# Performance work log

Hardware: AMD Instinct MI355X
Metric: run time of the kernel (lower is better)

Reference implementation:

```python
import jax, jax.numpy as jnp
import numpy as np

D_MODEL = 2048
N_HEADS = 16
D_HEAD = D_MODEL // N_HEADS
D_FF = 8192
EPS = 1e-6
ROPE_BASE = 10000.0


def rmsnorm(x, g):
    return x * jax.lax.rsqrt(jnp.mean(x * x, axis=-1, keepdims=True) + EPS) * g


def rotate_half(x):
    x1, x2 = jnp.split(x, 2, axis=-1)
    return jnp.concatenate((-x2, x1), axis=-1)


def rope_tables(T):
    inv_freq = 1.0 / (ROPE_BASE ** (jnp.arange(0, D_HEAD, 2, dtype=jnp.float32) / D_HEAD))
    freqs = jnp.arange(T, dtype=jnp.float32)[:, None] * inv_freq[None, :]  # [T, D_HEAD//2]
    emb = jnp.concatenate((freqs, freqs), axis=-1)  # [T, D_HEAD]
    return jnp.cos(emb), jnp.sin(emb)


def setup_inputs() -> dict:
    key = jax.random.key(0)
    ks = jax.random.split(key, 6)
    std = 0.02
    x = jax.random.normal(ks[0], (2, 2048, D_MODEL), dtype=jnp.float32)
    # weights stored (in, out) so forward is x @ W
    w_qkv = jax.random.normal(ks[1], (D_MODEL, 3 * D_MODEL), dtype=jnp.float32) * std
    w_out = jax.random.normal(ks[2], (D_MODEL, D_MODEL), dtype=jnp.float32) * std
    w_g = jax.random.normal(ks[3], (D_MODEL, D_FF), dtype=jnp.float32) * std
    w_u = jax.random.normal(ks[4], (D_MODEL, D_FF), dtype=jnp.float32) * std
    w_o = jax.random.normal(ks[5], (D_FF, D_MODEL), dtype=jnp.float32) * std
    g1 = jnp.ones((D_MODEL,), dtype=jnp.float32)
    g2 = jnp.ones((D_MODEL,), dtype=jnp.float32)
    return {"x": x, "w_qkv": w_qkv, "w_out": w_out, "g1": g1, "g2": g2,
            "w_g": w_g, "w_u": w_u, "w_o": w_o}


def reference(x, w_qkv, w_out, g1, g2, w_g, w_u, w_o):
    B, T, D = x.shape
    H, dh = N_HEADS, D_HEAD
    scale = dh ** -0.5

    h = rmsnorm(x, g1)
    qkv = h @ w_qkv  # [B, T, 3D]
    q, k, v = jnp.split(qkv, 3, axis=-1)
    # [B, H, T, dh]
    q = q.reshape(B, T, H, dh).transpose(0, 2, 1, 3)
    k = k.reshape(B, T, H, dh).transpose(0, 2, 1, 3)
    v = v.reshape(B, T, H, dh).transpose(0, 2, 1, 3)

    cos, sin = rope_tables(T)  # [T, dh] each
    cos = cos[None, None]
    sin = sin[None, None]
    q = q * cos + rotate_half(q) * sin
    k = k * cos + rotate_half(k) * sin

    scores = jnp.einsum('bhqd,bhkd->bhqk', q, k) * scale
    causal = jnp.arange(T)[None, :] <= jnp.arange(T)[:, None]  # [T, T]
    scores = jnp.where(causal[None, None], scores, -jnp.inf)
    attn = jax.nn.softmax(scores, axis=-1)
    ctx = jnp.einsum('bhqk,bhkd->bhqd', attn, v)  # [B, H, T, dh]
    ctx = ctx.transpose(0, 2, 1, 3).reshape(B, T, D)
    x = x + ctx @ w_out

    h = rmsnorm(x, g2)
    x = x + (jax.nn.silu(h @ w_g) * (h @ w_u)) @ w_o
    return x
```

## Files before the change

### kernel.cpp

```cpp
#include <hip/hip_runtime.h>

typedef __bf16 bf16x8 __attribute__((ext_vector_type(8)));
typedef float f32x4 __attribute__((ext_vector_type(4)));
typedef unsigned short u16x8 __attribute__((ext_vector_type(8)));

#define B_SZ 2
#define T_SEQ 2048
#define D_MODEL 2048
#define N_HEADS 16
#define D_HEAD 128
#define D_FF 8192
#define BT (B_SZ * T_SEQ)
#define NT (T_SEQ / 64)

__device__ __forceinline__ unsigned short f2bf(float f) {
  unsigned int u = __builtin_bit_cast(unsigned int, f);
  u += 0x7FFFu + ((u >> 16) & 1u);
  return (unsigned short)(u >> 16);
}
__device__ __forceinline__ float bf2f(unsigned short h) {
  unsigned int u = ((unsigned int)h) << 16;
  return __builtin_bit_cast(float, u);
}

__device__ __forceinline__ void load_lds16(const void* g, void* l) {
  __builtin_amdgcn_global_load_lds(
      (const __attribute__((address_space(1))) unsigned int*)g,
      (__attribute__((address_space(3))) unsigned int*)l, 16, 0, 0);
}

__global__ __launch_bounds__(256) void transpose_cast_kernel(
    const float* __restrict__ in, unsigned short* __restrict__ out, int R, int C) {
  __shared__ float tile[32][33];
  const int tx = threadIdx.x, ty = threadIdx.y;
  const int c0 = blockIdx.x * 32, r0 = blockIdx.y * 32;
#pragma unroll
  for (int i = 0; i < 4; ++i)
    tile[ty + 8 * i][tx] = in[(long)(r0 + ty + 8 * i) * C + c0 + tx];
  __syncthreads();
#pragma unroll
  for (int i = 0; i < 4; ++i)
    out[(long)(c0 + ty + 8 * i) * R + r0 + tx] = f2bf(tile[tx][ty + 8 * i]);
}

__global__ __launch_bounds__(256) void rmsnorm_cast_kernel(
    const float* __restrict__ x, const float* __restrict__ gw,
    unsigned short* __restrict__ out) {
  const int row = blockIdx.x;
  const int tid = threadIdx.x;
  const float* xr = x + (long)row * D_MODEL;
  float4 a = *(const float4*)(xr + tid * 8);
  float4 b = *(const float4*)(xr + tid * 8 + 4);
  float ss = a.x * a.x + a.y * a.y + a.z * a.z + a.w * a.w +
             b.x * b.x + b.y * b.y + b.z * b.z + b.w * b.w;
#pragma unroll
  for (int d = 1; d < 64; d <<= 1) ss += __shfl_xor(ss, d);
  __shared__ float part[4];
  if ((tid & 63) == 0) part[tid >> 6] = ss;
  __syncthreads();
  ss = part[0] + part[1] + part[2] + part[3];
  const float rs = rsqrtf(ss * (1.0f / D_MODEL) + 1e-6f);
  float4 g0 = *(const float4*)(gw + tid * 8);
  float4 g1 = *(const float4*)(gw + tid * 8 + 4);
  ushort4 o0, o1;
  o0.x = f2bf(a.x * rs * g0.x); o0.y = f2bf(a.y * rs * g0.y);
  o0.z = f2bf(a.z * rs * g0.z); o0.w = f2bf(a.w * rs * g0.w);
  o1.x = f2bf(b.x * rs * g1.x); o1.y = f2bf(b.y * rs * g1.y);
  o1.z = f2bf(b.z * rs * g1.z); o1.w = f2bf(b.w * rs * g1.w);
  unsigned short* op = out + (long)row * D_MODEL + tid * 8;
  *(ushort4*)op = o0;
  *(ushort4*)(op + 4) = o1;
}

template <int EPI>
__global__ __launch_bounds__(256) void gemm_bt_kernel(
    const unsigned short* __restrict__ A, const unsigned short* __restrict__ Bt,
    void* __restrict__ Cout, const void* __restrict__ aux,
    int M, int N, int K, int lda, int ldb, int ldc) {
  __shared__ unsigned short As[128 * 32];
  __shared__ unsigned short Bs[128 * 32];
  const int tid = threadIdx.x;
  const int w = tid >> 6, lane = tid & 63, g = lane >> 4, c = lane & 15;
  const int m0 = blockIdx.y * 128, n0 = blockIdx.x * 128;
  const int wm = (w >> 1) * 64, wn = (w & 1) * 64;
  const int srow = lane >> 2;
  const int scol = (lane & 3) * 8;
  const int ch0 = w * 2;
  f32x4 acc[4][4] = {};
  const int nkt = K >> 5;
  const unsigned short* Abase = A + (long)m0 * lda + scol;
  const unsigned short* Bbase = Bt + (long)n0 * ldb + scol;
  for (int kt = 0; kt < nkt; ++kt) {
    __syncthreads();
#pragma unroll
    for (int i = 0; i < 2; ++i) {
      const int ch = ch0 + i;
      load_lds16(Abase + (long)(ch * 16 + srow) * lda + kt * 32, &As[ch * 512]);
      load_lds16(Bbase + (long)(ch * 16 + srow) * ldb + kt * 32, &Bs[ch * 512]);
    }
    __syncthreads();
    bf16x8 fa[4], fb[4];
#pragma unroll
    for (int m = 0; m < 4; ++m)
      fa[m] = *(const bf16x8*)(As + (wm + m * 16 + c) * 32 + g * 8);
#pragma unroll
    for (int n = 0; n < 4; ++n)
      fb[n] = *(const bf16x8*)(Bs + (wn + n * 16 + c) * 32 + g * 8);
#pragma unroll
    for (int m = 0; m < 4; ++m)
#pragma unroll
      for (int n = 0; n < 4; ++n)
        acc[m][n] = __builtin_amdgcn_mfma_f32_16x16x32_bf16(fa[m], fb[n], acc[m][n], 0, 0, 0);
  }
#pragma unroll
  for (int m = 0; m < 4; ++m) {
#pragma unroll
    for (int r = 0; r < 4; ++r) {
      const int row = m0 + wm + m * 16 + 4 * g + r;
#pragma unroll
      for (int n = 0; n < 4; ++n) {
        const int col = n0 + wn + n * 16 + c;
        const long idx = (long)row * ldc + col;
        float v = acc[m][n][r];
        if constexpr (EPI == 0) {
          ((unsigned short*)Cout)[idx] = f2bf(v);
        } else if constexpr (EPI == 1) {
          ((float*)Cout)[idx] = v + ((const float*)aux)[idx];
        } else {
          const float u = bf2f(((const unsigned short*)aux)[idx]);
          const float s = v / (1.0f + __expf(-v));
          ((unsigned short*)Cout)[idx] = f2bf(s * u);
        }
      }
    }
  }
}

template <int EPI, int WM, int WN, int FM, int FN>
__global__ __launch_bounds__(WM * WN * 64, 2) void gemm_ks_kernel(
    const unsigned short* __restrict__ A, const unsigned short* __restrict__ Bt,
    void* __restrict__ Cout, const void* __restrict__ aux,
    int M, int N, int K, int lda, int ldb, int ldc, int cm, int cn) {
  constexpr int THREADS = WM * WN * 64;
  constexpr int BM = WM * FM * 16;
  constexpr int BN = WN * FN * 16;
  constexpr int ASLOT = BM * 32;
  constexpr int BSLOT = BN * 32;
  constexpr int RPR = THREADS / 4;
  __shared__ unsigned short As[4 * ASLOT];
  __shared__ unsigned short Bs[4 * BSLOT];

  const int tid = threadIdx.x;
  const int lane = tid & 63, g = lane >> 4, c = lane & 15;
  const int w = tid >> 6, wr = w / WN, wc = w % WN;

  const int nbn = N / BN;
  const int bid = (int)blockIdx.x;
  const int xcd = bid & 7, idx = bid >> 3;
  const int chn = nbn / cn;
  const int crow = xcd / chn, ccol = xcd % chn;
  const int mr = idx / cn, nc2 = idx % cn;
  const int m0 = (crow * cm + mr) * BM;
  const int n0 = (ccol * cn + nc2) * BN;

  const int nks = K >> 5;
  const int srow = tid >> 2;
  const int kq8 = (tid & 3) * 8;
  const unsigned short* A_ = A + (long)m0 * lda;
  const unsigned short* B_ = Bt + (long)n0 * ldb;

  auto stage = [&](int s) {
    const int slot = s & 3;
    const long kofs = (long)s * 32 + kq8;
#pragma unroll
    for (int j = 0; j < BM / RPR; ++j)
      load_lds16(A_ + (long)(j * RPR + srow) * lda + kofs,
                 &As[slot * ASLOT + (j * THREADS + tid) * 8]);
#pragma unroll
    for (int j = 0; j < BN / RPR; ++j)
      load_lds16(B_ + (long)(j * RPR + srow) * ldb + kofs,
                 &Bs[slot * BSLOT + (j * THREADS + tid) * 8]);
  };

  f32x4 acc[FM][FN] = {};

  stage(0);
  if (nks > 1) stage(1);
  if (nks > 2) stage(2);
  asm volatile("s_waitcnt vmcnt(8)" ::: "memory");
  __builtin_amdgcn_sched_barrier(0);
  __builtin_amdgcn_s_barrier();

  for (int s = 0; s < nks; ++s) {
    const int slot = s & 3;
    const unsigned short* Ap = &As[slot * ASLOT] + (wr * FM * 16 + c) * 32 + g * 8;
    const unsigned short* Bp = &Bs[slot * BSLOT] + (wc * FN * 16 + c) * 32 + g * 8;
    bf16x8 fa[FM], fb[FN];
#pragma unroll
    for (int fm = 0; fm < FM; ++fm) fa[fm] = *(const bf16x8*)(Ap + fm * 512);
#pragma unroll
    for (int fn = 0; fn < FN; ++fn) fb[fn] = *(const bf16x8*)(Bp + fn * 512);
    if (s + 3 < nks) stage(s + 3);
    __builtin_amdgcn_s_setprio(1);
#pragma unroll
    for (int fm = 0; fm < FM; ++fm)
#pragma unroll
      for (int fn = 0; fn < FN; ++fn)
        acc[fm][fn] = __builtin_amdgcn_mfma_f32_16x16x32_bf16(fa[fm], fb[fn], acc[fm][fn], 0, 0, 0);
    __builtin_amdgcn_s_setprio(0);
    if (s + 1 == nks) break;
    if (s <= nks - 4)
      asm volatile("s_waitcnt vmcnt(8)" ::: "memory");
    else if (s == nks - 3)
      asm volatile("s_waitcnt vmcnt(4)" ::: "memory");
    else
      asm volatile("s_waitcnt vmcnt(0)" ::: "memory");
    __builtin_amdgcn_sched_barrier(0);
    __builtin_amdgcn_s_barrier();
  }

#pragma unroll
  for (int fm = 0; fm < FM; ++fm) {
#pragma unroll
    for (int r = 0; r < 4; ++r) {
      const int row = m0 + wr * FM * 16 + fm * 16 + 4 * g + r;
#pragma unroll
      for (int fn = 0; fn < FN; ++fn) {
        const int col = n0 + wc * FN * 16 + fn * 16 + c;
        const long idx2 = (long)row * ldc + col;
        float v = acc[fm][fn][r];
        if constexpr (EPI == 0) {
          ((unsigned short*)Cout)[idx2] = f2bf(v);
        } else if constexpr (EPI == 1) {
          ((float*)Cout)[idx2] = v + ((const float*)aux)[idx2];
        } else {
          const float u = bf2f(((const unsigned short*)aux)[idx2]);
          const float sg = v / (1.0f + __expf(-v));
          ((unsigned short*)Cout)[idx2] = f2bf(sg * u);
        }
      }
    }
  }
}

__global__ void rope_tables_kernel(float* __restrict__ cost, float* __restrict__ sint) {
  const int idx = blockIdx.x * 256 + threadIdx.x;
  const int t = idx >> 6, i = idx & 63;
  const float invf = powf(10000.0f, -(float)i * (1.0f / 64.0f));
  const float ang = (float)t * invf;
  cost[idx] = cosf(ang);
  sint[idx] = sinf(ang);
}

__global__ __launch_bounds__(256) void rope_apply_kernel(
    unsigned short* __restrict__ qkv, const float* __restrict__ cost,
    const float* __restrict__ sint) {
  const long idx = (long)blockIdx.x * 256 + threadIdx.x;
  const int i = idx & 63;
  const int h = (idx >> 6) & 15;
  const int qk = (idx >> 10) & 1;
  const int row = idx >> 11;
  const int t = row & (T_SEQ - 1);
  unsigned short* p = qkv + (long)row * (3 * D_MODEL) + qk * D_MODEL + h * D_HEAD + i;
  const float a = bf2f(p[0]);
  const float b = bf2f(p[64]);
  const float cv = cost[t * 64 + i];
  const float sv = sint[t * 64 + i];
  p[0] = f2bf(a * cv - b * sv);
  p[64] = f2bf(b * cv + a * sv);
}

__global__ __launch_bounds__(256) void vtrans_kernel(
    const unsigned short* __restrict__ qkv, unsigned short* __restrict__ vt) {
  __shared__ unsigned short tile[32][33];
  const int tx = threadIdx.x, ty = threadIdx.y;
  const int t0 = blockIdx.x * 32, d0 = blockIdx.y * 32;
  const int bh = blockIdx.z;
  const int b = bh >> 4, h = bh & 15;
#pragma unroll
  for (int i = 0; i < 4; ++i)
    tile[ty + 8 * i][tx] =
        qkv[(long)(b * T_SEQ + t0 + ty + 8 * i) * (3 * D_MODEL) + 2 * D_MODEL + h * D_HEAD + d0 + tx];
  __syncthreads();
#pragma unroll
  for (int i = 0; i < 4; ++i)
    vt[((long)bh * D_HEAD + d0 + ty + 8 * i) * T_SEQ + t0 + tx] = tile[tx][ty + 8 * i];
}

__global__ __launch_bounds__(256) void attn_kernel(
    const unsigned short* __restrict__ qkv, const unsigned short* __restrict__ vt,
    unsigned short* __restrict__ ctx) {
  __shared__ unsigned short Ks[2][64 * 128];
  __shared__ unsigned short Vs[2][128 * 64];
  const int h = blockIdx.y, b = blockIdx.z;
  const int tid = threadIdx.x;
  const int w = tid >> 6, lane = tid & 63, g = lane >> 4, c = lane & 15;
  const float scale = 0.08838834764831845f;
  const int srcA = (2 * (g & 1)) * 16 + c;
  const int srcB = srcA + 16;
  const bool hi = (g >> 1) != 0;
  const int bh = b * N_HEADS + h;

  const int ssk = (tid & 15) ^ ((tid >> 4) & 7);
  const int ssv = (tid & 7) ^ ((tid >> 3) & 7);
  const unsigned short* Kg = qkv + (long)b * T_SEQ * 3 * D_MODEL + D_MODEL + (long)h * D_HEAD;
  const unsigned short* Vg = vt + (long)bh * D_HEAD * T_SEQ;

  auto stage = [&](int kv0, int bufi) {
#pragma unroll
    for (int i = 0; i < 4; ++i) {
      const int rowk = i * 16 + (tid >> 4);
      load_lds16(Kg + (long)(kv0 + rowk) * (3 * D_MODEL) + ssk * 8,
                 &Ks[bufi][(i * 256 + tid) * 8]);
    }
#pragma unroll
    for (int i = 0; i < 4; ++i) {
      const int rowv = i * 32 + (tid >> 3);
      load_lds16(Vg + (long)rowv * T_SEQ + kv0 + ssv * 8,
                 &Vs[bufi][(i * 256 + tid) * 8]);
    }
  };

  const int cs7 = c & 7;

  for (int pass = 0; pass < 2; ++pass) {
    const int qt = pass ? (NT - 1 - blockIdx.x) : blockIdx.x;
    const int q = qt * 64 + w * 16 + c;

    bf16x8 fq[4];
    const long rowQ = (long)(b * T_SEQ + q) * (3 * D_MODEL) + h * D_HEAD;
#pragma unroll
    for (int ks = 0; ks < 4; ++ks)
      fq[ks] = *(const bf16x8*)(qkv + rowQ + ks * 32 + g * 8);

    f32x4 o[8] = {};
    float mrun = -INFINITY, ell = 0.0f;

    stage(0, 0);
    asm volatile("s_waitcnt vmcnt(0)" ::: "memory");
    __syncthreads();
    int buf = 0;

    for (int kt = 0; kt <= qt; ++kt) {
      const int kv0 = kt * 64;
      if (kt < qt) stage(kv0 + 64, buf ^ 1);

      f32x4 s[4] = {};
#pragma unroll
      for (int fm = 0; fm < 4; ++fm) {
        const unsigned short* kr = &Ks[buf][(fm * 16 + c) * 128];
#pragma unroll
        for (int ks = 0; ks < 4; ++ks) {
          bf16x8 ak = *(const bf16x8*)(kr + ((ks * 4 + g) ^ cs7) * 8);
          s[fm] = __builtin_amdgcn_mfma_f32_16x16x32_bf16(ak, fq[ks], s[fm], 0, 0, 0);
        }
      }
      float pmax = -INFINITY;
      const bool diag = (kt == qt);
#pragma unroll
      for (int fm = 0; fm < 4; ++fm)
#pragma unroll
        for (int r = 0; r < 4; ++r) {
          float sv = s[fm][r] * scale;
          if (diag) {
            const int kp = kv0 + fm * 16 + 4 * g + r;
            if (kp > q) sv = -INFINITY;
          }
          s[fm][r] = sv;
          pmax = fmaxf(pmax, sv);
        }
      pmax = fmaxf(pmax, __shfl_xor(pmax, 16));
      pmax = fmaxf(pmax, __shfl_xor(pmax, 32));
      const float mnew = fmaxf(mrun, pmax);
      const float resc = __expf(mrun - mnew);
      mrun = mnew;
      float rowsum = 0.0f;
#pragma unroll
      for (int fm = 0; fm < 4; ++fm)
#pragma unroll
        for (int r = 0; r < 4; ++r) {
          const float p = __expf(s[fm][r] - mnew);
          s[fm][r] = p;
          rowsum += p;
        }
      rowsum += __shfl_xor(rowsum, 16);
      rowsum += __shfl_xor(rowsum, 32);
      ell = ell * resc + rowsum;
#pragma unroll
      for (int fm = 0; fm < 8; ++fm) o[fm] *= resc;

      bf16x8 pb[2];
#pragma unroll
      for (int k2 = 0; k2 < 2; ++k2) {
        float va[4], vb[4];
#pragma unroll
        for (int r = 0; r < 4; ++r) {
          const float t0 = __shfl(s[k2 * 2][r], srcA);
          const float t1 = __shfl(s[k2 * 2 + 1][r], srcA);
          va[r] = hi ? t1 : t0;
          const float u0 = __shfl(s[k2 * 2][r], srcB);
          const float u1 = __shfl(s[k2 * 2 + 1][r], srcB);
          vb[r] = hi ? u1 : u0;
        }
        bf16x8 pv;
        pv[0] = (__bf16)va[0]; pv[1] = (__bf16)va[1];
        pv[2] = (__bf16)va[2]; pv[3] = (__bf16)va[3];
        pv[4] = (__bf16)vb[0]; pv[5] = (__bf16)vb[1];
        pv[6] = (__bf16)vb[2]; pv[7] = (__bf16)vb[3];
        pb[k2] = pv;
      }
#pragma unroll
      for (int fm = 0; fm < 8; ++fm) {
        const unsigned short* vr = &Vs[buf][(fm * 16 + c) * 64];
#pragma unroll
        for (int k2 = 0; k2 < 2; ++k2) {
          bf16x8 av = *(const bf16x8*)(vr + ((k2 * 4 + g) ^ cs7) * 8);
          o[fm] = __builtin_amdgcn_mfma_f32_16x16x32_bf16(av, pb[k2], o[fm], 0, 0, 0);
        }
      }
      asm volatile("s_waitcnt vmcnt(0)" ::: "memory");
      __syncthreads();
      buf ^= 1;
    }

    const float inv = 1.0f / ell;
    unsigned short* outp = ctx + (long)(b * T_SEQ + q) * D_MODEL + h * D_HEAD;
#pragma unroll
    for (int fm = 0; fm < 8; ++fm) {
      ushort4 pk;
      pk.x = f2bf(o[fm][0] * inv);
      pk.y = f2bf(o[fm][1] * inv);
      pk.z = f2bf(o[fm][2] * inv);
      pk.w = f2bf(o[fm][3] * inv);
      *(ushort4*)(outp + fm * 16 + 4 * g) = pk;
    }
  }
}

extern "C" void kernel_launch(void* const* d_in, const int* in_sizes, int n_in,
                              void* d_out, int out_size, void* d_ws, size_t ws_size,
                              hipStream_t stream) {
  const float* x = (const float*)d_in[0];
  const float* w_qkv = (const float*)d_in[1];
  const float* w_out = (const float*)d_in[2];
  const float* g1 = (const float*)d_in[3];
  const float* g2 = (const float*)d_in[4];
  const float* w_g = (const float*)d_in[5];
  const float* w_u = (const float*)d_in[6];
  const float* w_o = (const float*)d_in[7];
  float* out = (float*)d_out;

  char* ws = (char*)d_ws;
  size_t off = 0;
  auto take = [&](size_t bytes) {
    char* p = ws + off;
    off += (bytes + 255) & ~(size_t)255;
    return p;
  };

  char* Wreg = take((size_t)3 * D_FF * D_MODEL * 2);
  unsigned short* wTqkv = (unsigned short*)Wreg;
  unsigned short* wTout = (unsigned short*)(Wreg + (size_t)3 * D_MODEL * D_MODEL * 2);
  unsigned short* wTg = (unsigned short*)Wreg;
  unsigned short* wTu = (unsigned short*)(Wreg + (size_t)D_FF * D_MODEL * 2);
  unsigned short* wTo = (unsigned short*)(Wreg + (size_t)2 * D_FF * D_MODEL * 2);

  const size_t qkv_b = (size_t)BT * 3 * D_MODEL * 2;
  const size_t vt_b = (size_t)B_SZ * N_HEADS * D_HEAD * T_SEQ * 2;
  const size_t ctx_b = (size_t)BT * D_MODEL * 2;
  char* AR = take(qkv_b + vt_b + ctx_b);
  unsigned short* qkvb = (unsigned short*)AR;
  unsigned short* vtb = (unsigned short*)(AR + qkv_b);
  unsigned short* ctxb = (unsigned short*)(AR + qkv_b + vt_b);
  unsigned short* gbuf = (unsigned short*)AR;
  unsigned short* ubuf = (unsigned short*)(AR + (size_t)BT * (D_FF / 2) * 2);

  float* x1 = (float*)take((size_t)BT * D_MODEL * 4);
  unsigned short* hb = (unsigned short*)take((size_t)BT * D_MODEL * 2);
  float* cost = (float*)take((size_t)T_SEQ * 64 * 4);
  float* sint = (float*)take((size_t)T_SEQ * 64 * 4);

  const dim3 tb(32, 8);

  transpose_cast_kernel<<<dim3(3 * D_MODEL / 32, D_MODEL / 32), tb, 0, stream>>>(w_qkv, wTqkv, D_MODEL, 3 * D_MODEL);
  transpose_cast_kernel<<<dim3(D_MODEL / 32, D_MODEL / 32), tb, 0, stream>>>(w_out, wTout, D_MODEL, D_MODEL);
  rope_tables_kernel<<<T_SEQ * 64 / 256, 256, 0, stream>>>(cost, sint);

  rmsnorm_cast_kernel<<<BT, 256, 0, stream>>>(x, g1, hb);
  gemm_ks_kernel<0, 2, 4, 8, 4><<<384, 512, 0, stream>>>(
      hb, wTqkv, qkvb, nullptr, BT, 3 * D_MODEL, D_MODEL, D_MODEL, D_MODEL, 3 * D_MODEL, 8, 6);
  rope_apply_kernel<<<(BT * N_HEADS * 64 * 2) / 256, 256, 0, stream>>>(qkvb, cost, sint);
  vtrans_kernel<<<dim3(T_SEQ / 32, D_HEAD / 32, B_SZ * N_HEADS), tb, 0, stream>>>(qkvb, vtb);
  attn_kernel<<<dim3(NT / 2, N_HEADS, B_SZ), 256, 0, stream>>>(qkvb, vtb, ctxb);
  gemm_ks_kernel<1, 2, 2, 4, 4><<<512, 256, 0, stream>>>(
      ctxb, wTout, x1, x, BT, D_MODEL, D_MODEL, D_MODEL, D_MODEL, D_MODEL, 8, 8);

  transpose_cast_kernel<<<dim3(D_FF / 32, D_MODEL / 32), tb, 0, stream>>>(w_g, wTg, D_MODEL, D_FF);
  transpose_cast_kernel<<<dim3(D_FF / 32, D_MODEL / 32), tb, 0, stream>>>(w_u, wTu, D_MODEL, D_FF);
  transpose_cast_kernel<<<dim3(D_MODEL / 32, D_FF / 32), tb, 0, stream>>>(w_o, wTo, D_FF, D_MODEL);
  rmsnorm_cast_kernel<<<BT, 256, 0, stream>>>(x1, g2, hb);

  const int NH = D_FF / 2;
  for (int half = 0; half < 2; ++half) {
    const unsigned short* wTu_h = wTu + (size_t)half * NH * D_MODEL;
    const unsigned short* wTg_h = wTg + (size_t)half * NH * D_MODEL;
    const unsigned short* wTo_h = wTo + (size_t)half * NH;
    gemm_ks_kernel<0, 2, 4, 8, 4><<<256, 512, 0, stream>>>(
        hb, wTu_h, ubuf, nullptr, BT, NH, D_MODEL, D_MODEL, D_MODEL, NH, 4, 8);
    gemm_ks_kernel<2, 2, 4, 8, 4><<<256, 512, 0, stream>>>(
        hb, wTg_h, gbuf, ubuf, BT, NH, D_MODEL, D_MODEL, D_MODEL, NH, 4, 8);
    gemm_ks_kernel<1, 2, 2, 4, 4><<<512, 256, 0, stream>>>(
        gbuf, wTo_h, out, (half == 0) ? x1 : out, BT, D_MODEL, NH, NH, D_FF, D_MODEL, 8, 8);
  }
}
```

Baseline: 804.5 us.

## Add double-buffered 256x256 GEMM kernel with swizzled LDS for QKV and MLP

Replaces the unused gemm_bt kernel with a new 256x256-tile GEMM that uses 512 threads and a BK=64 double-buffered LDS pipeline. It prefetches two stages ahead with explicit vmcnt waits, XOR-swizzles LDS columns to avoid bank conflicts, and raises wave priority around the MFMA block. The QKV, up-projection and gate-projection GEMMs now call it with XCD-aware block mapping. The goal is to hide global load latency and reuse more data per tile, at the cost of 128 KB of LDS per block and heavy register pressure from 32 accumulators.

New measurement: 804.6 us. Within noise of the previous version (+0.0%).

```diff
diff --git a/kernel.cpp b/kernel.cpp
--- a/kernel.cpp
+++ b/kernel.cpp
@@ -73,55 +73,104 @@
 }
 
 template <int EPI>
-__global__ __launch_bounds__(256) void gemm_bt_kernel(
+__global__ __launch_bounds__(512, 2) void gemm256_kernel(
     const unsigned short* __restrict__ A, const unsigned short* __restrict__ Bt,
     void* __restrict__ Cout, const void* __restrict__ aux,
-    int M, int N, int K, int lda, int ldb, int ldc) {
-  __shared__ unsigned short As[128 * 32];
-  __shared__ unsigned short Bs[128 * 32];
+    int M, int N, int K, int lda, int ldb, int ldc, int cm, int cn) {
+  __shared__ unsigned short As[2][16384];
+  __shared__ unsigned short Bs[2][16384];
   const int tid = threadIdx.x;
-  const int w = tid >> 6, lane = tid & 63, g = lane >> 4, c = lane & 15;
-  const int m0 = blockIdx.y * 128, n0 = blockIdx.x * 128;
-  const int wm = (w >> 1) * 64, wn = (w & 1) * 64;
-  const int srow = lane >> 2;
-  const int scol = (lane & 3) * 8;
-  const int ch0 = w * 2;
-  f32x4 acc[4][4] = {};
-  const int nkt = K >> 5;
-  const unsigned short* Abase = A + (long)m0 * lda + scol;
-  const unsigned short* Bbase = Bt + (long)n0 * ldb + scol;
+  const int lane = tid & 63, g = lane >> 4, c = lane & 15;
+  const int w = tid >> 6, wr = w >> 2, wc = w & 3;
+
+  const int nbn = N >> 8;
+  const int bid = (int)blockIdx.x;
+  const int xcd = bid & 7, bidx = bid >> 3;
+  const int chn = nbn / cn;
+  const int crow = xcd / chn, ccol = xcd % chn;
+  const int m0 = (crow * cm + bidx / cn) << 8;
+  const int n0 = (ccol * cn + bidx % cn) << 8;
+
+  const int nkt = K >> 6;
+  const int L0 = tid, L1 = 512 + tid;
+  const int row0 = L0 >> 3, cs0 = ((L0 & 7) ^ (row0 & 7)) * 8;
+  const int row1 = L1 >> 3, cs1 = ((L1 & 7) ^ (row1 & 7)) * 8;
+  const int wbase = (tid & ~63) * 8;
+  const unsigned short* Abase = A + (long)m0 * lda;
+  const unsigned short* Bbase = Bt + (long)n0 * ldb;
+
+  auto stage = [&](int kt) {
+    const int bufi = kt & 1;
+    const long kofs = (long)kt * 64;
+#pragma unroll
+    for (int h = 0; h < 2; ++h) {
+      load_lds16(Abase + (long)(h * 128 + row0) * lda + kofs + cs0, &As[bufi][h * 8192 + wbase]);
+      load_lds16(Abase + (long)(h * 128 + row1) * lda + kofs + cs1, &As[bufi][h * 8192 + 4096 + wbase]);
+    }
+#pragma unroll
+    for (int h = 0; h < 2; ++h) {
+      load_lds16(Bbase + (long)(h * 128 + row0) * ldb + kofs + cs0, &Bs[bufi][h * 8192 + wbase]);
+      load_lds16(Bbase + (long)(h * 128 + row1) * ldb + kofs + cs1, &Bs[bufi][h * 8192 + 4096 + wbase]);
+    }
+  };
+
+  f32x4 acc[8][4] = {};
+  const int c7 = c & 7;
+
+  stage(0);
+  if (nkt > 1) stage(1);
+  asm volatile("s_waitcnt vmcnt(8)" ::: "memory");
+  __builtin_amdgcn_sched_barrier(0);
+  __builtin_amdgcn_s_barrier();
+
   for (int kt = 0; kt < nkt; ++kt) {
-    __syncthreads();
-#pragma unroll
-    for (int i = 0; i < 2; ++i) {
-      const int ch = ch0 + i;
-      load_lds16(Abase + (long)(ch * 16 + srow) * lda + kt * 32, &As[ch * 512]);
-      load_lds16(Bbase + (long)(ch * 16 + srow) * ldb + kt * 32, &Bs[ch * 512]);
-    }
-    __syncthreads();
-    bf16x8 fa[4], fb[4];
-#pragma unroll
-    for (int m = 0; m < 4; ++m)
-      fa[m] = *(const bf16x8*)(As + (wm + m * 16 + c) * 32 + g * 8);
-#pragma unroll
-    for (int n = 0; n < 4; ++n)
-      fb[n] = *(const bf16x8*)(Bs + (wn + n * 16 + c) * 32 + g * 8);
-#pragma unroll
-    for (int m = 0; m < 4; ++m)
-#pragma unroll
-      for (int n = 0; n < 4; ++n)
-        acc[m][n] = __builtin_amdgcn_mfma_f32_16x16x32_bf16(fa[m], fb[n], acc[m][n], 0, 0, 0);
+    const int bufi = kt & 1;
+    const unsigned short* Ap = &As[bufi][wr * 8192];
+    const unsigned short* Bp = &Bs[bufi][(wc >> 1) * 8192 + (wc & 1) * 4096];
+    bf16x8 fb[4][2], fa[8][2];
+#pragma unroll
+    for (int fn = 0; fn < 4; ++fn)
+#pragma unroll
+      for (int ks = 0; ks < 2; ++ks)
+        fb[fn][ks] = *(const bf16x8*)(Bp + (fn * 16 + c) * 64 + (((ks * 4 + g) ^ c7) * 8));
+#pragma unroll
+    for (int fm = 0; fm < 8; ++fm) {
+      const unsigned short* ar = Ap + (fm * 16 + c) * 64;
+      fa[fm][0] = *(const bf16x8*)(ar + ((g ^ c7) * 8));
+      fa[fm][1] = *(const bf16x8*)(ar + (((4 + g) ^ c7) * 8));
+    }
+    asm volatile("s_waitcnt lgkmcnt(0)" ::: "memory");
+    __builtin_amdgcn_sched_barrier(0);
+    __builtin_amdgcn_s_barrier();
+    if (kt + 2 < nkt) stage(kt + 2);
+    __builtin_amdgcn_s_setprio(1);
+#pragma unroll
+    for (int fm = 0; fm < 8; ++fm)
+#pragma unroll
+      for (int fn = 0; fn < 4; ++fn) {
+        acc[fm][fn] = __builtin_amdgcn_mfma_f32_16x16x32_bf16(fa[fm][0], fb[fn][0], acc[fm][fn], 0, 0, 0);
+        acc[fm][fn] = __builtin_amdgcn_mfma_f32_16x16x32_bf16(fa[fm][1], fb[fn][1], acc[fm][fn], 0, 0, 0);
+      }
+    __builtin_amdgcn_s_setprio(0);
+    if (kt + 1 == nkt) break;
+    if (kt + 2 < nkt)
+      asm volatile("s_waitcnt vmcnt(8)" ::: "memory");
+    else
+      asm volatile("s_waitcnt vmcnt(0)" ::: "memory");
+    __builtin_amdgcn_sched_barrier(0);
+    __builtin_amdgcn_s_barrier();
   }
-#pragma unroll
-  for (int m = 0; m < 4; ++m) {
+
+#pragma unroll
+  for (int fm = 0; fm < 8; ++fm) {
 #pragma unroll
     for (int r = 0; r < 4; ++r) {
-      const int row = m0 + wm + m * 16 + 4 * g + r;
-#pragma unroll
-      for (int n = 0; n < 4; ++n) {
-        const int col = n0 + wn + n * 16 + c;
+      const int row = m0 + wr * 128 + fm * 16 + 4 * g + r;
+#pragma unroll
+      for (int fn = 0; fn < 4; ++fn) {
+        const int col = n0 + wc * 64 + fn * 16 + c;
         const long idx = (long)row * ldc + col;
-        float v = acc[m][n][r];
+        float v = acc[fm][fn][r];
         if constexpr (EPI == 0) {
           ((unsigned short*)Cout)[idx] = f2bf(v);
         } else if constexpr (EPI == 1) {
@@ -487,7 +536,7 @@
   rope_tables_kernel<<<T_SEQ * 64 / 256, 256, 0, stream>>>(cost, sint);
 
   rmsnorm_cast_kernel<<<BT, 256, 0, stream>>>(x, g1, hb);
-  gemm_ks_kernel<0, 2, 4, 8, 4><<<384, 512, 0, stream>>>(
+  gemm256_kernel<0><<<384, 512, 0, stream>>>(
       hb, wTqkv, qkvb, nullptr, BT, 3 * D_MODEL, D_MODEL, D_MODEL, D_MODEL, 3 * D_MODEL, 8, 6);
   rope_apply_kernel<<<(BT * N_HEADS * 64 * 2) / 256, 256, 0, stream>>>(qkvb, cost, sint);
   vtrans_kernel<<<dim3(T_SEQ / 32, D_HEAD / 32, B_SZ * N_HEADS), tb, 0, stream>>>(qkvb, vtb);
@@ -505,9 +554,9 @@
     const unsigned short* wTu_h = wTu + (size_t)half * NH * D_MODEL;
     const unsigned short* wTg_h = wTg + (size_t)half * NH * D_MODEL;
     const unsigned short* wTo_h = wTo + (size_t)half * NH;
-    gemm_ks_kernel<0, 2, 4, 8, 4><<<256, 512, 0, stream>>>(
+    gemm256_kernel<0><<<256, 512, 0, stream>>>(
         hb, wTu_h, ubuf, nullptr, BT, NH, D_MODEL, D_MODEL, D_MODEL, NH, 4, 8);
-    gemm_ks_kernel<2, 2, 4, 8, 4><<<256, 512, 0, stream>>>(
+    gemm256_kernel<2><<<256, 512, 0, stream>>>(
         hb, wTg_h, gbuf, ubuf, BT, NH, D_MODEL, D_MODEL, D_MODEL, NH, 4, 8);
     gemm_ks_kernel<1, 2, 2, 4, 4><<<512, 256, 0, stream>>>(
         gbuf, wTo_h, out, (half == 0) ? x1 : out, BT, D_MODEL, NH, NH, D_FF, D_MODEL, 8, 8);
```
